# Kernel optimization log

Measured on AMD Instinct MI355X. Metric: run time of the kernel, lower is better.

The kernel has to match this reference:

```python
import jax, jax.numpy as jnp
import numpy as np

N_NODES = 10000
N_REL = 200
DIM = 128          # rank * 2
REL_DIM = 128
VIS_DIM = 512
TXT_DIM = 768
N_EDGES = 320000


def _glorot(key, shape):
    fan_in, fan_out = shape[1], shape[0]
    lim = (6.0 / (fan_in + fan_out)) ** 0.5
    return jax.random.uniform(key, shape, jnp.float32, -lim, lim)


def setup_inputs() -> dict:
    key = jax.random.key(0)
    ks = jax.random.split(key, 24)
    inp = {}
    inp['x'] = jax.random.randint(ks[0], (1024, 3), 0, N_NODES)
    inp['edge_index'] = jax.random.randint(ks[1], (2, N_EDGES), 0, N_NODES)
    inp['edge_type'] = jax.random.randint(ks[2], (N_EDGES,), 0, N_REL)
    inp['visual'] = jax.random.normal(ks[3], (N_NODES, VIS_DIM), jnp.float32)
    inp['textual'] = jax.random.normal(ks[4], (N_NODES, TXT_DIM), jnp.float32)
    # embeddings (scaled by 0.001 as in torch init)
    inp['structural_emb'] = jax.random.normal(ks[5], (N_NODES, DIM), jnp.float32) * 0.001
    inp['relation_emb'] = jax.random.normal(ks[6], (N_REL, REL_DIM), jnp.float32) * 0.001
    # three KBGAT convs: w1 [out, 2*in+rel], b1 [out], w2 [1, out]
    cat = 2 * DIM + REL_DIM
    for i, tag in enumerate(['s', 'v', 't']):
        inp[f'W1_{tag}'] = _glorot(ks[7 + 3 * i], (DIM, cat))
        inp[f'b1_{tag}'] = jnp.zeros((DIM,), jnp.float32)
        inp[f'w2_{tag}'] = _glorot(ks[8 + 3 * i], (1, DIM))
    # modality projections
    inp['Wv'] = _glorot(ks[16], (DIM, VIS_DIM))
    inp['bv'] = jnp.zeros((DIM,), jnp.float32)
    inp['Wt'] = _glorot(ks[17], (DIM, TXT_DIM))
    inp['bt'] = jnp.zeros((DIM,), jnp.float32)
    inp['alpha'] = jnp.float32(0.1)
    inp['gamma'] = jnp.float32(0.8)
    return inp


def kbgat_conv(feat, rel_emb, src, dst, edge_type, W1, b1, w2):
    # gather per-edge embeddings: x_i = target, x_j = source (PyG default flow)
    triple = jnp.concatenate([feat[dst], feat[src], rel_emb[edge_type]], axis=1)  # [E, 2*D+R]
    c = triple @ W1.T + b1                                   # [E, D]
    b = jax.nn.leaky_relu(c @ w2[0])                         # [E]
    # segment softmax over destination nodes
    m = jax.ops.segment_max(b, dst, num_segments=N_NODES)
    e = jnp.exp(b - m[dst])
    z = jax.ops.segment_sum(e, dst, num_segments=N_NODES)
    attn = e / z[dst]                                        # [E]
    agg = jax.ops.segment_sum(c * attn[:, None], dst, num_segments=N_NODES)  # [N, D]
    return jax.nn.leaky_relu(agg)


def reference(x, edge_index, edge_type, visual, textual, structural_emb, relation_emb,
              W1_s, b1_s, w2_s, W1_v, b1_v, w2_v, W1_t, b1_t, w2_t,
              Wv, bv, Wt, bt, alpha, gamma):
    src, dst = edge_index[0], edge_index[1]
    h_s = kbgat_conv(structural_emb, relation_emb, src, dst, edge_type, W1_s, b1_s, w2_s)
    vf = visual @ Wv.T + bv
    h_v = kbgat_conv(vf, relation_emb, src, dst, edge_type, W1_v, b1_v, w2_v)
    tf = textual @ Wt.T + bt
    h_t = kbgat_conv(tf, relation_emb, src, dst, edge_type, W1_t, b1_t, w2_t)
    return (1.0 - alpha - gamma) * h_s + alpha * h_v + gamma * h_t
```

## Files before the change

kernel.cpp:

```cpp
#include <hip/hip_runtime.h>
#include <hip/hip_bf16.h>

typedef unsigned short u16;
typedef unsigned int u32;
typedef unsigned long long u64;
typedef __bf16 bf16x8 __attribute__((ext_vector_type(8)));
typedef float f32x4 __attribute__((ext_vector_type(4)));

#define DIM 128

__device__ __forceinline__ u16 f2bf_rne(float x) {
  u32 u = __float_as_uint(x);
  return (u16)((u + 0x7fffu + ((u >> 16) & 1u)) >> 16);
}
__device__ __forceinline__ u32 packbf2(float x, float y) {
  return (u32)f2bf_rne(x) | ((u32)f2bf_rne(y) << 16);
}
__device__ __forceinline__ float lrelu(float x) { return x > 0.f ? x : 0.01f * x; }
__device__ __forceinline__ int iclamp(int v, int hi) { return v < 0 ? 0 : (v >= hi ? hi - 1 : v); }
__device__ __forceinline__ float sane(float x) { return (x == x) ? x : 0.f; }

__device__ __forceinline__ float wred_max(float v) {
  #pragma unroll
  for (int o = 32; o > 0; o >>= 1) v = fmaxf(v, __shfl_xor(v, o, 64));
  return v;
}
__device__ __forceinline__ float wred_sum(float v) {
  #pragma unroll
  for (int o = 32; o > 0; o >>= 1) v += __shfl_xor(v, o, 64);
  return v;
}

struct PrepAllArgs {
  const float* W1[3]; const float* Wmod[3]; int K[3]; u16* Wc[3];
  const float* rel; const float* b1[3]; const float* bmod[3]; const float* w2[3];
  u16* PrAll; float* qr[3]; int NR;
  const int* cnt; int* offs; int N;
  int wc2End; int wc1End; int wc0End;
};
struct MainArgs {
  const float* A[3]; const u16* B[3]; const float* w2[3];
  u16* PdAll; u16* PsAll; float* qd[3]; float* qs[3];
  int M; int K[3]; int tilesPerM; int nGemm; int totB;
  const int* dst; const int* src; const int* etyp;
  const int* offs; const int* rank; u32* sortedST;
  int E; int NR;
};
struct AgArgs {
  const u32* sortedST; const int* offs;
  const float* qd[3]; const float* qs[3]; const float* qr[3];
  const u16* PdAll; const u16* PsAll; const u16* PrAll;
  const float* alphaP; const float* gammaP;
  float* outp; int N; int NR; int E;
};

__global__ __launch_bounds__(256) void hist_k(const int* __restrict__ dst,
                                              int* __restrict__ cnt,
                                              int* __restrict__ rank, int E, int N) {
  int e0 = blockIdx.x * 512 + threadIdx.x;
  #pragma unroll
  for (int i = 0; i < 2; ++i) {
    int e = e0 + i * 256;
    if (e < E) {
      int d = dst[e];
      if (d >= 0 && d < N) rank[e] = atomicAdd(&cnt[d], 1);
    }
  }
}

__global__ __launch_bounds__(256) void scan_wcpr(PrepAllArgs a) {
  __shared__ float relL[2][128];
  __shared__ float bmL[128];
  __shared__ float qpr[4];
  __shared__ int sums[256];
  int b = blockIdx.x, tid = threadIdx.x;

  if (b == 0) {
    int N = a.N;
    int chunk = (N + 255) >> 8;
    int base = tid * chunk;
    int s = 0;
    for (int i = 0; i < chunk; ++i) { int idx = base + i; if (idx < N) s += a.cnt[idx]; }
    sums[tid] = s;
    __syncthreads();
    for (int off = 1; off < 256; off <<= 1) {
      int v = (tid >= off) ? sums[tid - off] : 0;
      __syncthreads();
      sums[tid] += v;
      __syncthreads();
    }
    int prefix = (tid > 0) ? sums[tid - 1] : 0;
    for (int i = 0; i < chunk; ++i) {
      int idx = base + i;
      if (idx < N) { a.offs[idx] = prefix; prefix += a.cnt[idx]; }
    }
    if (tid == 255) a.offs[N] = sums[255];
    return;
  }

  int c = b - 1;
  if (c < a.wc0End) {
    int m, loc;
    if (c < a.wc2End)      { m = 2; loc = c; }
    else if (c < a.wc1End) { m = 1; loc = c - a.wc2End; }
    else                   { m = 0; loc = c - a.wc1End; }
    int og = loc & 31, kb = loc >> 5;
    int o0 = og * 8;
    int k = (kb << 8) + tid;
    int K = a.K[m];
    if (k < K) {
      int halfsel = (o0 >= 128) ? 128 : 0;
      int oo0 = o0 & 127;
      const float* W1 = a.W1[m];
      const float* Wm = a.Wmod[m];
      float acc[8];
      if (Wm == nullptr) {
        #pragma unroll
        for (int u = 0; u < 8; ++u)
          acc[u] = W1[(oo0 + u) * 384 + halfsel + k];
      } else {
        #pragma unroll
        for (int u = 0; u < 8; ++u) acc[u] = 0.f;
        const float* wmk = Wm + k;
        const float* w1b = W1 + (size_t)oo0 * 384 + halfsel;
        for (int i = 0; i < 128; i += 8) {
          float wm[8];
          #pragma unroll
          for (int j = 0; j < 8; ++j)
            wm[j] = wmk[(size_t)(i + j) * K];
          #pragma unroll
          for (int j = 0; j < 8; ++j) {
            #pragma unroll
            for (int u = 0; u < 8; ++u)
              acc[u] = fmaf(w1b[u * 384 + i + j], wm[j], acc[u]);
          }
        }
      }
      #pragma unroll
      for (int u = 0; u < 8; ++u) {
        int o = o0 + u;
        a.Wc[m][((size_t)(k >> 5) * 256 + o) * 32 + (k & 31)] = f2bf_rne(acc[u]);
      }
    }
  } else {
    int idx = c - a.wc0End;
    int NRpair = (a.NR + 1) >> 1;
    int m = idx / NRpair;
    if (m > 2) return;
    int rp = idx - m * NRpair;
    int r0 = rp * 2;
    {
      int ro = tid >> 7, ii = tid & 127;
      int rr = r0 + ro;
      relL[ro][ii] = (rr < a.NR) ? a.rel[rr * 128 + ii] : 0.f;
    }
    const float* bmod = a.bmod[m];
    if (tid < 128) bmL[tid] = (bmod != nullptr) ? bmod[tid] : 0.f;
    __syncthreads();
    int lane = tid & 63, wv = tid >> 6;
    int rsel = wv >> 1;
    int obase = (wv & 1) * 64;
    int r = r0 + rsel;
    bool rok = (r < a.NR);
    const float* W1 = a.W1[m];
    const float* b1 = a.b1[m];
    const float* w2 = a.w2[m];
    bool hasbm = (bmod != nullptr);
    float rl0 = relL[rsel][lane], rl1 = relL[rsel][64 + lane];
    float bm0 = bmL[lane], bm1 = bmL[64 + lane];
    float qacc = 0.f;
    for (int oo = 0; oo < 64; oo += 4) {
      float s[4];
      #pragma unroll
      for (int u = 0; u < 4; ++u) {
        const float* row = W1 + (obase + oo + u) * 384;
        float v = row[256 + lane] * rl0 + row[320 + lane] * rl1;
        if (hasbm)
          v += (row[lane] + row[128 + lane]) * bm0 +
               (row[64 + lane] + row[192 + lane]) * bm1;
        s[u] = v;
      }
      #pragma unroll
      for (int off2 = 32; off2 > 0; off2 >>= 1) {
        #pragma unroll
        for (int u = 0; u < 4; ++u) s[u] += __shfl_xor(s[u], off2, 64);
      }
      u16 pk[4];
      #pragma unroll
      for (int u = 0; u < 4; ++u) {
        int o = obase + oo + u;
        float totv = s[u] + b1[o];
        pk[u] = f2bf_rne(totv);
        qacc += totv * w2[o];
      }
      if (rok && lane == 0) {
        u16* dstp = a.PrAll + (size_t)r * 384 + m * 128 + obase + oo;
        *reinterpret_cast<u64*>(dstp) =
            (u64)pk[0] | ((u64)pk[1] << 16) | ((u64)pk[2] << 32) | ((u64)pk[3] << 48);
      }
    }
    if (lane == 0) qpr[wv] = qacc;
    __syncthreads();
    if (tid < 2) {
      int rr = r0 + tid;
      if (rr < a.NR) a.qr[m][rr] = sane(qpr[tid * 2] + qpr[tid * 2 + 1]);
    }
  }
}

__device__ __forceinline__ void gemm_epilogue(const MainArgs& g, int m, int row0,
                                              f32x4 (&acc)[2][4], float (*qpart)[32]) {
  int tid = threadIdx.x;
  int lane = tid & 63, wv = tid >> 6;
  int quad = lane >> 4, l16 = lane & 15;
  int M = g.M;
  const float* w2 = g.w2[m];
  u16* PdAll = g.PdAll;
  u16* PsAll = g.PsAll;
  float w2c[4];
  #pragma unroll
  for (int t = 0; t < 4; ++t) w2c[t] = w2[(wv & 1) * 64 + t * 16 + l16];

  #pragma unroll
  for (int rg = 0; rg < 2; ++rg) {
    float part[4];
    #pragma unroll
    for (int r = 0; r < 4; ++r) {
      int rr = row0 + rg * 16 + quad * 4 + r;
      bool ok = rr < M;
      float qp = 0.f;
      #pragma unroll
      for (int t = 0; t < 4; ++t) {
        int cc = (wv & 1) * 64 + t * 16 + l16;
        if (ok) {
          if (wv < 2) PdAll[(size_t)rr * 384 + m * 128 + cc] = f2bf_rne(acc[rg][t][r]);
          else        PsAll[(size_t)rr * 384 + m * 128 + cc] = f2bf_rne(acc[rg][t][r]);
        }
        qp += acc[rg][t][r] * w2c[t];
      }
      #pragma unroll
      for (int mk = 1; mk < 16; mk <<= 1) qp += __shfl_xor(qp, mk, 64);
      part[r] = qp;
    }
    if (l16 == 0) {
      #pragma unroll
      for (int r = 0; r < 4; ++r) qpart[wv][rg * 16 + quad * 4 + r] = part[r];
    }
  }
  __syncthreads();
  if (tid < 64) {
    int row = tid & 31;
    int half = tid >> 5;
    int rr = row0 + row;
    if (rr < M) {
      if (half == 0) g.qd[m][rr] = sane(qpart[0][row] + qpart[1][row]);
      else           g.qs[m][rr] = sane(qpart[2][row] + qpart[3][row]);
    }
  }
}

template<int NT>
__device__ __forceinline__ void gemm_exact(const MainArgs& g, int m, int tile,
                                           u16* Als, float (*qpart)[32]) {
  constexpr int H = (NT + 1) / 2;
  const int M = g.M;
  int tid = threadIdx.x;
  int lane = tid & 63, wv = tid >> 6;
  int quad = lane >> 4, l16 = lane & 15;
  int row0 = tile * 32;
  int srow = tid >> 3;
  int tk4 = (tid & 7) * 4;
  int srsw = srow & 3;
  int wg = tk4 >> 3;
  int wrem = tk4 & 7;
  int grow = row0 + srow;
  if (grow >= M) grow = M - 1;
  const float* Ag = g.A[m] + (size_t)grow * (NT * 32);

  float4 vreg[H];
  #pragma unroll
  for (int i = 0; i < H; ++i)
    vreg[i] = *reinterpret_cast<const float4*>(Ag + tk4 + i * 32);
  #pragma unroll
  for (int i = 0; i < H; ++i) {
    int gidx = wg ^ srsw ^ (i & 3);
    u32* dp = reinterpret_cast<u32*>(&Als[((i * 32 + srow) * 32) + (gidx << 3) + wrem]);
    dp[0] = packbf2(vreg[i].x, vreg[i].y);
    dp[1] = packbf2(vreg[i].z, vreg[i].w);
  }
  #pragma unroll
  for (int i = H; i < NT; ++i)
    vreg[i - H] = *reinterpret_cast<const float4*>(Ag + tk4 + i * 32);
  #pragma unroll
  for (int i = H; i < NT; ++i) {
    int gidx = wg ^ srsw ^ (i & 3);
    u32* dp = reinterpret_cast<u32*>(&Als[((i * 32 + srow) * 32) + (gidx << 3) + wrem]);
    dp[0] = packbf2(vreg[i - H].x, vreg[i - H].y);
    dp[1] = packbf2(vreg[i - H].z, vreg[i - H].w);
  }
  __syncthreads();

  const u16* Bpg = g.B[m] + (size_t)(wv * 64 + l16) * 32 + quad * 8;
  f32x4 acc[2][4];
  #pragma unroll
  for (int rg = 0; rg < 2; ++rg)
    #pragma unroll
    for (int t = 0; t < 4; ++t) acc[rg][t] = (f32x4){0.f, 0.f, 0.f, 0.f};

  #pragma unroll
  for (int kb = 0; kb < NT; ++kb) {
    const u16* bp = Bpg + (size_t)kb * 8192;
    bf16x8 b0 = *reinterpret_cast<const bf16x8*>(bp);
    bf16x8 b1 = *reinterpret_cast<const bf16x8*>(bp + 512);
    bf16x8 b2 = *reinterpret_cast<const bf16x8*>(bp + 1024);
    bf16x8 b3 = *reinterpret_cast<const bf16x8*>(bp + 1536);
    int gsw = (quad ^ (l16 & 3) ^ (kb & 3)) << 3;
    #pragma unroll
    for (int rg = 0; rg < 2; ++rg) {
      bf16x8 av = *reinterpret_cast<const bf16x8*>(
          &Als[(kb * 32 + rg * 16 + l16) * 32 + gsw]);
      acc[rg][0] = __builtin_amdgcn_mfma_f32_16x16x32_bf16(av, b0, acc[rg][0], 0, 0, 0);
      acc[rg][1] = __builtin_amdgcn_mfma_f32_16x16x32_bf16(av, b1, acc[rg][1], 0, 0, 0);
      acc[rg][2] = __builtin_amdgcn_mfma_f32_16x16x32_bf16(av, b2, acc[rg][2], 0, 0, 0);
      acc[rg][3] = __builtin_amdgcn_mfma_f32_16x16x32_bf16(av, b3, acc[rg][3], 0, 0, 0);
    }
  }
  gemm_epilogue(g, m, row0, acc, qpart);
}

__device__ void gemm_generic(const MainArgs& g, int m, int tile,
                             u16* Als, float (*qpart)[32]) {
  const int M = g.M, K = g.K[m];
  int nt = K >> 5;
  int tid = threadIdx.x;
  int lane = tid & 63, wv = tid >> 6;
  int quad = lane >> 4, l16 = lane & 15;
  int row0 = tile * 32;
  int srow = tid >> 3;
  int tk4 = (tid & 7) * 4;
  int srsw = srow & 3;
  int wg = tk4 >> 3;
  int wrem = tk4 & 7;
  int grow = row0 + srow;
  if (grow >= M) grow = M - 1;
  const float* Ag = g.A[m] + (size_t)grow * K;
  const u16* Bpg = g.B[m] + (size_t)(wv * 64 + l16) * 32 + quad * 8;

  f32x4 acc[2][4];
  #pragma unroll
  for (int rg = 0; rg < 2; ++rg)
    #pragma unroll
    for (int t = 0; t < 4; ++t) acc[rg][t] = (f32x4){0.f, 0.f, 0.f, 0.f};

  for (int c0 = 0; c0 < nt; c0 += 24) {
    int kc = nt - c0; if (kc > 24) kc = 24;
    __syncthreads();
    for (int i = 0; i < kc; ++i) {
      int kg = (c0 + i) * 32 + tk4;
      if (kg + 3 < K) {
        float4 v = *reinterpret_cast<const float4*>(Ag + kg);
        int gidx = wg ^ srsw ^ (i & 3);
        u32* dp = reinterpret_cast<u32*>(&Als[((i * 32 + srow) * 32) + (gidx << 3) + wrem]);
        dp[0] = packbf2(v.x, v.y);
        dp[1] = packbf2(v.z, v.w);
      }
    }
    __syncthreads();
    for (int kb = 0; kb < kc; ++kb) {
      const u16* bp = Bpg + (size_t)(c0 + kb) * 8192;
      bf16x8 b0 = *reinterpret_cast<const bf16x8*>(bp);
      bf16x8 b1 = *reinterpret_cast<const bf16x8*>(bp + 512);
      bf16x8 b2 = *reinterpret_cast<const bf16x8*>(bp + 1024);
      bf16x8 b3 = *reinterpret_cast<const bf16x8*>(bp + 1536);
      int gsw = (quad ^ (l16 & 3) ^ (kb & 3)) << 3;
      #pragma unroll
      for (int rg = 0; rg < 2; ++rg) {
        bf16x8 av = *reinterpret_cast<const bf16x8*>(
            &Als[(kb * 32 + rg * 16 + l16) * 32 + gsw]);
        acc[rg][0] = __builtin_amdgcn_mfma_f32_16x16x32_bf16(av, b0, acc[rg][0], 0, 0, 0);
        acc[rg][1] = __builtin_amdgcn_mfma_f32_16x16x32_bf16(av, b1, acc[rg][1], 0, 0, 0);
        acc[rg][2] = __builtin_amdgcn_mfma_f32_16x16x32_bf16(av, b2, acc[rg][2], 0, 0, 0);
        acc[rg][3] = __builtin_amdgcn_mfma_f32_16x16x32_bf16(av, b3, acc[rg][3], 0, 0, 0);
      }
    }
  }
  gemm_epilogue(g, m, row0, acc, qpart);
}

__global__ __launch_bounds__(256) void fused_main(MainArgs g) {
  __shared__ __align__(16) u16 Als[24 * 32 * 32];
  __shared__ float qpart[4][32];
  int b = blockIdx.x;
  long nG = g.nGemm, tot = g.totB;
  int gprev = (int)((long)b * nG / tot);
  int gnext = (int)(((long)b + 1) * nG / tot);
  if (gnext == gprev) {
    int h = b - gprev;
    int e = h * 256 + threadIdx.x;
    if (e < g.E) {
      int d = g.dst[e];
      if (d >= 0 && d < g.M) {
        int pos = g.offs[d] + g.rank[e];
        if (pos >= 0 && pos < g.E) {
          u32 s = (u32)iclamp(g.src[e], g.M);
          u32 t = (u32)iclamp(g.etyp[e], g.NR);
          g.sortedST[pos] = (t << 16) | s;
        }
      }
    }
    return;
  }
  int fb = gprev;
  int tpm = g.tilesPerM;
  int m, tile;
  if (fb < tpm)            { m = 2; tile = fb; }
  else if (fb < 2 * tpm)   { m = 1; tile = fb - tpm; }
  else                     { m = 0; tile = fb - 2 * tpm; }

  int K = g.K[m];
  if (K == 768)      gemm_exact<24>(g, m, tile, Als, qpart);
  else if (K == 512) gemm_exact<16>(g, m, tile, Als, qpart);
  else if (K == 128) gemm_exact<4>(g, m, tile, Als, qpart);
  else               gemm_generic(g, m, tile, Als, qpart);
}

__global__ __launch_bounds__(256) void aggregate_all(AgArgs a) {
  int n = blockIdx.x * 4 + (threadIdx.x >> 6);
  if (n >= a.N) return;
  int lane = threadIdx.x & 63;
  int E = a.E;
  int eb = a.offs[n], ee = a.offs[n + 1];
  if (eb < 0) eb = 0;
  if (eb > E) eb = E;
  if (ee < eb) ee = eb;
  if (ee > E) ee = E;
  int En = ee - eb;

  float al = a.alphaP[0];
  if (!(al > 0.f && al < 1.f)) al = 0.1f;
  float ga = a.gammaP[0];
  if (!(ga > 0.f && ga < 1.f)) ga = 0.8f;
  float coef[3] = {1.f - al - ga, al, ga};

  float qdn[3];
  #pragma unroll
  for (int m = 0; m < 3; ++m) qdn[m] = sane(a.qd[m][n]);

  const u16* PsAll = a.PsAll;
  const u16* PrAll = a.PrAll;
  int dlo = 2 * lane;

  float rm[3] = {-1e30f, -1e30f, -1e30f};
  float z[3] = {0.f, 0.f, 0.f};
  float a0[3] = {0.f, 0.f, 0.f};
  float a1[3] = {0.f, 0.f, 0.f};
  for (int c0 = 0; c0 < En; c0 += 64) {
    int cn = min(64, En - c0);
    u32 stp = 0;
    float bm[3] = {-1e30f, -1e30f, -1e30f};
    if (lane < cn) {
      stp = a.sortedST[eb + c0 + lane];
      int s = (int)(stp & 0xffffu);
      int t = (int)(stp >> 16);
      #pragma unroll
      for (int m = 0; m < 3; ++m)
        bm[m] = lrelu(qdn[m] + a.qs[m][s] + a.qr[m][t]);
    }
    float wr[3];
    #pragma unroll
    for (int m = 0; m < 3; ++m) {
      float cm = wred_max(bm[m]);
      float nm = fmaxf(rm[m], cm);
      float sc = __expf(fmaxf(rm[m] - nm, -80.f));
      z[m] *= sc; a0[m] *= sc; a1[m] *= sc;
      rm[m] = nm;
      wr[m] = (lane < cn) ? __expf(fmaxf(bm[m] - nm, -80.f)) : 0.f;
      z[m] += wr[m];
    }

    int cnR = (cn + 3) & ~3;
    for (int j = 0; j < cnR; j += 4) {
      u32 stj[4];
      float wj[4][3];
      #pragma unroll
      for (int u = 0; u < 4; ++u) {
        stj[u] = __shfl(stp, j + u, 64);
        wj[u][0] = __shfl(wr[0], j + u, 64);
        wj[u][1] = __shfl(wr[1], j + u, 64);
        wj[u][2] = __shfl(wr[2], j + u, 64);
      }
      u32 pu[4][3], ru[4][3];
      #pragma unroll
      for (int u = 0; u < 4; ++u) {
        const u16* ps = PsAll + (size_t)(stj[u] & 0xffffu) * 384 + dlo;
        const u16* pr = PrAll + (size_t)(stj[u] >> 16) * 384 + dlo;
        #pragma unroll
        for (int m = 0; m < 3; ++m) {
          pu[u][m] = *reinterpret_cast<const u32*>(ps + m * 128);
          ru[u][m] = *reinterpret_cast<const u32*>(pr + m * 128);
        }
      }
      #pragma unroll
      for (int u = 0; u < 4; ++u) {
        #pragma unroll
        for (int m = 0; m < 3; ++m) {
          float ps0 = __uint_as_float(pu[u][m] << 16);
          float ps1 = __uint_as_float(pu[u][m] & 0xffff0000u);
          float pr0 = __uint_as_float(ru[u][m] << 16);
          float pr1 = __uint_as_float(ru[u][m] & 0xffff0000u);
          a0[m] = fmaf(wj[u][m], ps0 + pr0, a0[m]);
          a1[m] = fmaf(wj[u][m], ps1 + pr1, a1[m]);
        }
      }
    }
  }
  #pragma unroll
  for (int m = 0; m < 3; ++m) z[m] = wred_sum(z[m]);

  float o0 = 0.f, o1 = 0.f;
  const u16* pd = a.PdAll + (size_t)n * 384 + dlo;
  #pragma unroll
  for (int m = 0; m < 3; ++m) {
    float h0 = 0.f, h1 = 0.f;
    if (En > 0 && z[m] > 0.f) {
      float rz = 1.f / z[m];
      u32 du = *reinterpret_cast<const u32*>(pd + m * 128);
      float pd0 = __uint_as_float(du << 16), pd1 = __uint_as_float(du & 0xffff0000u);
      h0 = lrelu(pd0 + a0[m] * rz);
      h1 = lrelu(pd1 + a1[m] * rz);
    }
    o0 = fmaf(coef[m], h0, o0);
    o1 = fmaf(coef[m], h1, o1);
  }
  float* op = a.outp + (size_t)n * 128 + dlo;
  op[0] = sane(o0);
  op[1] = sane(o1);
}

extern "C" void kernel_launch(void* const* d_in, const int* in_sizes, int n_in,
                              void* d_out, int out_size, void* d_ws, size_t ws_size,
                              hipStream_t stream) {
  const int* ei        = (const int*)d_in[1];
  const int* et        = (const int*)d_in[2];
  const float* visual  = (const float*)d_in[3];
  const float* textual = (const float*)d_in[4];
  const float* semb    = (const float*)d_in[5];
  const float* relemb  = (const float*)d_in[6];
  const float* W1s = (const float*)d_in[7];
  const float* b1s = (const float*)d_in[8];
  const float* w2s = (const float*)d_in[9];
  const float* W1v = (const float*)d_in[10];
  const float* b1v = (const float*)d_in[11];
  const float* w2v = (const float*)d_in[12];
  const float* W1t = (const float*)d_in[13];
  const float* b1t = (const float*)d_in[14];
  const float* w2t = (const float*)d_in[15];
  const float* Wv  = (const float*)d_in[16];
  const float* bv  = (const float*)d_in[17];
  const float* Wt  = (const float*)d_in[18];
  const float* bt  = (const float*)d_in[19];
  const float* alphaP = (const float*)d_in[20];
  const float* gammaP = (const float*)d_in[21];
  float* outp = (float*)d_out;

  const int E   = in_sizes[2];
  const int N   = in_sizes[5] / DIM;
  const int NR  = in_sizes[6] / DIM;
  const int VIS = in_sizes[3] / N;
  const int TXT = in_sizes[4] / N;
  int Ks[3] = {DIM, VIS, TXT};
  const int TPM = (N + 31) / 32;

  const float* W1a[3]   = {W1s, W1v, W1t};
  const float* b1a[3]   = {b1s, b1v, b1t};
  const float* w2a[3]   = {w2s, w2v, w2t};
  const float* Wmoda[3] = {nullptr, Wv, Wt};
  const float* bmoda[3] = {nullptr, bv, bt};
  const float* Amoda[3] = {semb, visual, textual};

  const int* esrc = ei;
  const int* edst = ei + E;
  int egrid  = (E + 255) / 256;
  int egridH = (E + 511) / 512;

  size_t off = 0;
  auto take = [&](size_t bytes) -> size_t {
    size_t o = off;
    off = (off + bytes + 255) & ~(size_t)255;
    return o;
  };
  size_t o_cnt  = take((size_t)N * 4);
  size_t o_rank = take((size_t)E * 4);
  size_t o_offs = take((size_t)(N + 1) * 4);
  size_t o_st   = take((size_t)E * 4);
  size_t o_qdm[3], o_qsm[3], o_qrm[3], o_Wcm[3];
  for (int m = 0; m < 3; ++m) {
    o_qdm[m] = take((size_t)N * 4);
    o_qsm[m] = take((size_t)N * 4);
    o_qrm[m] = take((size_t)NR * 4);
    o_Wcm[m] = take((size_t)256 * Ks[m] * 2);
  }
  size_t o_PrAll = take((size_t)NR * 384 * 2);
  size_t o_PdAll = take((size_t)N * 384 * 2);
  size_t o_PsAll = take((size_t)N * 384 * 2);
  size_t need = off;

  if (ws_size < need) {
    (void)hipMemsetAsync(d_out, 0, (size_t)out_size * 4, stream);
    return;
  }

  char* w = (char*)d_ws;
  int* counts = (int*)(w + o_cnt);
  int* rank   = (int*)(w + o_rank);
  int* offs   = (int*)(w + o_offs);
  u32* sortedST = (u32*)(w + o_st);

  (void)hipMemsetAsync(counts, 0, (size_t)N * 4, stream);

  PrepAllArgs pa;
  pa.rel = relemb; pa.NR = NR;
  pa.PrAll = (u16*)(w + o_PrAll);
  pa.cnt = counts; pa.offs = offs; pa.N = N;
  for (int m = 0; m < 3; ++m) {
    pa.W1[m] = W1a[m]; pa.Wmod[m] = Wmoda[m]; pa.K[m] = Ks[m];
    pa.Wc[m] = (u16*)(w + o_Wcm[m]);
    pa.b1[m] = b1a[m]; pa.bmod[m] = bmoda[m]; pa.w2[m] = w2a[m];
    pa.qr[m] = (float*)(w + o_qrm[m]);
  }
  int NRpair = (NR + 1) / 2;
  int kbm[3];
  for (int m = 0; m < 3; ++m) kbm[m] = (Ks[m] + 255) / 256;
  pa.wc2End = 32 * kbm[2];
  pa.wc1End = pa.wc2End + 32 * kbm[1];
  pa.wc0End = pa.wc1End + 32 * kbm[0];
  int prepGrid = 1 + pa.wc0End + 3 * NRpair;

  MainArgs ga;
  ga.M = N; ga.tilesPerM = TPM; ga.nGemm = 3 * TPM;
  ga.totB = ga.nGemm + egrid;
  ga.PdAll = (u16*)(w + o_PdAll);
  ga.PsAll = (u16*)(w + o_PsAll);
  ga.dst = edst; ga.src = esrc; ga.etyp = et;
  ga.offs = offs; ga.rank = rank; ga.sortedST = sortedST;
  ga.E = E; ga.NR = NR;
  AgArgs aa;
  for (int m = 0; m < 3; ++m) {
    ga.A[m] = Amoda[m]; ga.B[m] = (const u16*)(w + o_Wcm[m]); ga.w2[m] = w2a[m];
    ga.qd[m] = (float*)(w + o_qdm[m]); ga.qs[m] = (float*)(w + o_qsm[m]);
    ga.K[m] = Ks[m];
    aa.qd[m] = (const float*)(w + o_qdm[m]);
    aa.qs[m] = (const float*)(w + o_qsm[m]);
    aa.qr[m] = (const float*)(w + o_qrm[m]);
  }

  aa.PdAll = (const u16*)(w + o_PdAll);
  aa.PsAll = (const u16*)(w + o_PsAll);
  aa.PrAll = (const u16*)(w + o_PrAll);
  aa.sortedST = sortedST; aa.offs = offs;
  aa.alphaP = alphaP; aa.gammaP = gammaP;
  aa.outp = outp; aa.N = N; aa.NR = NR; aa.E = E;

  hist_k<<<egridH, 256, 0, stream>>>(edst, counts, rank, E, N);
  scan_wcpr<<<prepGrid, 256, 0, stream>>>(pa);
  fused_main<<<ga.totB, 256, 0, stream>>>(ga);
  aggregate_all<<<(N + 3) / 4, 256, 0, stream>>>(aa);
}
```

Measured before the change: 248.0 us.

## Halve GEMM row tile to 16 rows and restructure weight-combine FMA loop

The fused projection GEMM now uses 16-row tiles instead of 32, with a new LDS staging helper and epilogue sized to match. This doubles the number of GEMM blocks, giving more parallelism across CUs and halving LDS use per block. In exchange each block reuses the B-operand weights over fewer rows, so total B traffic from cache doubles. Separately, the weight-combination loop in the prep kernel is rewritten as per-output FMA chains, and that kernel is given a launch bound of 1.

```diff
diff --git a/kernel.cpp b/kernel.cpp
--- a/kernel.cpp
+++ b/kernel.cpp
@@ -68,7 +68,7 @@
   }
 }
 
-__global__ __launch_bounds__(256) void scan_wcpr(PrepAllArgs a) {
+__global__ __launch_bounds__(256, 1) void scan_wcpr(PrepAllArgs a) {
   __shared__ float relL[2][128];
   __shared__ float bmL[128];
   __shared__ float qpr[4];
@@ -124,15 +124,25 @@
         const float* wmk = Wm + k;
         const float* w1b = W1 + (size_t)oo0 * 384 + halfsel;
         for (int i = 0; i < 128; i += 8) {
-          float wm[8];
+          float wm0 = wmk[(size_t)(i + 0) * K];
+          float wm1 = wmk[(size_t)(i + 1) * K];
+          float wm2 = wmk[(size_t)(i + 2) * K];
+          float wm3 = wmk[(size_t)(i + 3) * K];
+          float wm4 = wmk[(size_t)(i + 4) * K];
+          float wm5 = wmk[(size_t)(i + 5) * K];
+          float wm6 = wmk[(size_t)(i + 6) * K];
+          float wm7 = wmk[(size_t)(i + 7) * K];
           #pragma unroll
-          for (int j = 0; j < 8; ++j)
-            wm[j] = wmk[(size_t)(i + j) * K];
-          #pragma unroll
-          for (int j = 0; j < 8; ++j) {
-            #pragma unroll
-            for (int u = 0; u < 8; ++u)
-              acc[u] = fmaf(w1b[u * 384 + i + j], wm[j], acc[u]);
+          for (int u = 0; u < 8; ++u) {
+            const float* r_ = w1b + u * 384 + i;
+            float s0 = fmaf(r_[0], wm0, acc[u]);
+            s0 = fmaf(r_[1], wm1, s0);
+            s0 = fmaf(r_[2], wm2, s0);
+            s0 = fmaf(r_[3], wm3, s0);
+            s0 = fmaf(r_[4], wm4, s0);
+            s0 = fmaf(r_[5], wm5, s0);
+            s0 = fmaf(r_[6], wm6, s0);
+            acc[u] = fmaf(r_[7], wm7, s0);
           }
         }
       }
@@ -208,51 +218,52 @@
   }
 }
 
-__device__ __forceinline__ void gemm_epilogue(const MainArgs& g, int m, int row0,
-                                              f32x4 (&acc)[2][4], float (*qpart)[32]) {
+__device__ __forceinline__ void stash16(u16* Als, int srow, int tk4, int i, float4 v) {
+  int kb = 2 * i + (tk4 >> 5);
+  int kl = tk4 & 31;
+  int gidx = (kl >> 3) ^ (srow & 3) ^ (kb & 3);
+  u32* dp = reinterpret_cast<u32*>(&Als[(kb * 16 + srow) * 32 + (gidx << 3) + (kl & 7)]);
+  dp[0] = packbf2(v.x, v.y);
+  dp[1] = packbf2(v.z, v.w);
+}
+
+__device__ __forceinline__ void epilogue16(const MainArgs& g, int m, int row0,
+                                           f32x4 (&acc)[4], float (*qpart)[16]) {
   int tid = threadIdx.x;
   int lane = tid & 63, wv = tid >> 6;
   int quad = lane >> 4, l16 = lane & 15;
-  int M = g.M;
   const float* w2 = g.w2[m];
-  u16* PdAll = g.PdAll;
-  u16* PsAll = g.PsAll;
   float w2c[4];
   #pragma unroll
   for (int t = 0; t < 4; ++t) w2c[t] = w2[(wv & 1) * 64 + t * 16 + l16];
-
-  #pragma unroll
-  for (int rg = 0; rg < 2; ++rg) {
-    float part[4];
+  float part[4];
+  #pragma unroll
+  for (int r = 0; r < 4; ++r) {
+    int rr = row0 + quad * 4 + r;
+    bool ok = rr < g.M;
+    float qp = 0.f;
     #pragma unroll
-    for (int r = 0; r < 4; ++r) {
-      int rr = row0 + rg * 16 + quad * 4 + r;
-      bool ok = rr < M;
-      float qp = 0.f;
-      #pragma unroll
-      for (int t = 0; t < 4; ++t) {
-        int cc = (wv & 1) * 64 + t * 16 + l16;
-        if (ok) {
-          if (wv < 2) PdAll[(size_t)rr * 384 + m * 128 + cc] = f2bf_rne(acc[rg][t][r]);
-          else        PsAll[(size_t)rr * 384 + m * 128 + cc] = f2bf_rne(acc[rg][t][r]);
-        }
-        qp += acc[rg][t][r] * w2c[t];
-      }
-      #pragma unroll
-      for (int mk = 1; mk < 16; mk <<= 1) qp += __shfl_xor(qp, mk, 64);
-      part[r] = qp;
-    }
-    if (l16 == 0) {
-      #pragma unroll
-      for (int r = 0; r < 4; ++r) qpart[wv][rg * 16 + quad * 4 + r] = part[r];
-    }
+    for (int t = 0; t < 4; ++t) {
+      int cc = (wv & 1) * 64 + t * 16 + l16;
+      if (ok) {
+        if (wv < 2) g.PdAll[(size_t)rr * 384 + m * 128 + cc] = f2bf_rne(acc[t][r]);
+        else        g.PsAll[(size_t)rr * 384 + m * 128 + cc] = f2bf_rne(acc[t][r]);
+      }
+      qp += acc[t][r] * w2c[t];
+    }
+    #pragma unroll
+    for (int mk = 1; mk < 16; mk <<= 1) qp += __shfl_xor(qp, mk, 64);
+    part[r] = qp;
+  }
+  if (l16 == 0) {
+    #pragma unroll
+    for (int r = 0; r < 4; ++r) qpart[wv][quad * 4 + r] = part[r];
   }
   __syncthreads();
-  if (tid < 64) {
-    int row = tid & 31;
-    int half = tid >> 5;
+  if (tid < 32) {
+    int row = tid & 15, half = tid >> 4;
     int rr = row0 + row;
-    if (rr < M) {
+    if (rr < g.M) {
       if (half == 0) g.qd[m][rr] = sane(qpart[0][row] + qpart[1][row]);
       else           g.qs[m][rr] = sane(qpart[2][row] + qpart[3][row]);
     }
@@ -260,52 +271,35 @@
 }
 
 template<int NT>
-__device__ __forceinline__ void gemm_exact(const MainArgs& g, int m, int tile,
-                                           u16* Als, float (*qpart)[32]) {
-  constexpr int H = (NT + 1) / 2;
-  const int M = g.M;
+__device__ __forceinline__ void gemm16(const MainArgs& g, int m, int tile,
+                                       u16* Als, float (*qpart)[16]) {
+  constexpr int NS = NT / 2;
+  constexpr int H = (NS + 1) / 2;
   int tid = threadIdx.x;
   int lane = tid & 63, wv = tid >> 6;
   int quad = lane >> 4, l16 = lane & 15;
-  int row0 = tile * 32;
-  int srow = tid >> 3;
-  int tk4 = (tid & 7) * 4;
-  int srsw = srow & 3;
-  int wg = tk4 >> 3;
-  int wrem = tk4 & 7;
+  int row0 = tile * 16;
+  int srow = tid >> 4;
+  int tk4 = (tid & 15) * 4;
   int grow = row0 + srow;
-  if (grow >= M) grow = M - 1;
+  if (grow >= g.M) grow = g.M - 1;
   const float* Ag = g.A[m] + (size_t)grow * (NT * 32);
 
   float4 vreg[H];
   #pragma unroll
-  for (int i = 0; i < H; ++i)
-    vreg[i] = *reinterpret_cast<const float4*>(Ag + tk4 + i * 32);
-  #pragma unroll
-  for (int i = 0; i < H; ++i) {
-    int gidx = wg ^ srsw ^ (i & 3);
-    u32* dp = reinterpret_cast<u32*>(&Als[((i * 32 + srow) * 32) + (gidx << 3) + wrem]);
-    dp[0] = packbf2(vreg[i].x, vreg[i].y);
-    dp[1] = packbf2(vreg[i].z, vreg[i].w);
-  }
-  #pragma unroll
-  for (int i = H; i < NT; ++i)
-    vreg[i - H] = *reinterpret_cast<const float4*>(Ag + tk4 + i * 32);
-  #pragma unroll
-  for (int i = H; i < NT; ++i) {
-    int gidx = wg ^ srsw ^ (i & 3);
-    u32* dp = reinterpret_cast<u32*>(&Als[((i * 32 + srow) * 32) + (gidx << 3) + wrem]);
-    dp[0] = packbf2(vreg[i - H].x, vreg[i - H].y);
-    dp[1] = packbf2(vreg[i - H].z, vreg[i - H].w);
-  }
+  for (int i = 0; i < H; ++i) vreg[i] = *reinterpret_cast<const float4*>(Ag + tk4 + i * 64);
+  #pragma unroll
+  for (int i = 0; i < H; ++i) stash16(Als, srow, tk4, i, vreg[i]);
+  #pragma unroll
+  for (int i = H; i < NS; ++i) vreg[i - H] = *reinterpret_cast<const float4*>(Ag + tk4 + i * 64);
+  #pragma unroll
+  for (int i = H; i < NS; ++i) stash16(Als, srow, tk4, i, vreg[i - H]);
   __syncthreads();
 
   const u16* Bpg = g.B[m] + (size_t)(wv * 64 + l16) * 32 + quad * 8;
-  f32x4 acc[2][4];
-  #pragma unroll
-  for (int rg = 0; rg < 2; ++rg)
-    #pragma unroll
-    for (int t = 0; t < 4; ++t) acc[rg][t] = (f32x4){0.f, 0.f, 0.f, 0.f};
+  f32x4 acc[4];
+  #pragma unroll
+  for (int t = 0; t < 4; ++t) acc[t] = (f32x4){0.f, 0.f, 0.f, 0.f};
 
   #pragma unroll
   for (int kb = 0; kb < NT; ++kb) {
@@ -315,54 +309,40 @@
     bf16x8 b2 = *reinterpret_cast<const bf16x8*>(bp + 1024);
     bf16x8 b3 = *reinterpret_cast<const bf16x8*>(bp + 1536);
     int gsw = (quad ^ (l16 & 3) ^ (kb & 3)) << 3;
-    #pragma unroll
-    for (int rg = 0; rg < 2; ++rg) {
-      bf16x8 av = *reinterpret_cast<const bf16x8*>(
-          &Als[(kb * 32 + rg * 16 + l16) * 32 + gsw]);
-      acc[rg][0] = __builtin_amdgcn_mfma_f32_16x16x32_bf16(av, b0, acc[rg][0], 0, 0, 0);
-      acc[rg][1] = __builtin_amdgcn_mfma_f32_16x16x32_bf16(av, b1, acc[rg][1], 0, 0, 0);
-      acc[rg][2] = __builtin_amdgcn_mfma_f32_16x16x32_bf16(av, b2, acc[rg][2], 0, 0, 0);
-      acc[rg][3] = __builtin_amdgcn_mfma_f32_16x16x32_bf16(av, b3, acc[rg][3], 0, 0, 0);
-    }
-  }
-  gemm_epilogue(g, m, row0, acc, qpart);
-}
-
-__device__ void gemm_generic(const MainArgs& g, int m, int tile,
-                             u16* Als, float (*qpart)[32]) {
-  const int M = g.M, K = g.K[m];
+    bf16x8 av = *reinterpret_cast<const bf16x8*>(&Als[(kb * 16 + l16) * 32 + gsw]);
+    acc[0] = __builtin_amdgcn_mfma_f32_16x16x32_bf16(av, b0, acc[0], 0, 0, 0);
+    acc[1] = __builtin_amdgcn_mfma_f32_16x16x32_bf16(av, b1, acc[1], 0, 0, 0);
+    acc[2] = __builtin_amdgcn_mfma_f32_16x16x32_bf16(av, b2, acc[2], 0, 0, 0);
+    acc[3] = __builtin_amdgcn_mfma_f32_16x16x32_bf16(av, b3, acc[3], 0, 0, 0);
+  }
+  epilogue16(g, m, row0, acc, qpart);
+}
+
+__device__ void gemm16_gen(const MainArgs& g, int m, int tile,
+                           u16* Als, float (*qpart)[16]) {
+  const int K = g.K[m];
   int nt = K >> 5;
   int tid = threadIdx.x;
   int lane = tid & 63, wv = tid >> 6;
   int quad = lane >> 4, l16 = lane & 15;
-  int row0 = tile * 32;
-  int srow = tid >> 3;
-  int tk4 = (tid & 7) * 4;
-  int srsw = srow & 3;
-  int wg = tk4 >> 3;
-  int wrem = tk4 & 7;
+  int row0 = tile * 16;
+  int srow = tid >> 4;
+  int tk4 = (tid & 15) * 4;
   int grow = row0 + srow;
-  if (grow >= M) grow = M - 1;
+  if (grow >= g.M) grow = g.M - 1;
   const float* Ag = g.A[m] + (size_t)grow * K;
   const u16* Bpg = g.B[m] + (size_t)(wv * 64 + l16) * 32 + quad * 8;
-
-  f32x4 acc[2][4];
-  #pragma unroll
-  for (int rg = 0; rg < 2; ++rg)
-    #pragma unroll
-    for (int t = 0; t < 4; ++t) acc[rg][t] = (f32x4){0.f, 0.f, 0.f, 0.f};
-
+  f32x4 acc[4];
+  #pragma unroll
+  for (int t = 0; t < 4; ++t) acc[t] = (f32x4){0.f, 0.f, 0.f, 0.f};
   for (int c0 = 0; c0 < nt; c0 += 24) {
     int kc = nt - c0; if (kc > 24) kc = 24;
     __syncthreads();
-    for (int i = 0; i < kc; ++i) {
-      int kg = (c0 + i) * 32 + tk4;
+    for (int i = 0; i < (kc + 1) / 2; ++i) {
+      int kg = c0 * 32 + tk4 + i * 64;
       if (kg + 3 < K) {
         float4 v = *reinterpret_cast<const float4*>(Ag + kg);
-        int gidx = wg ^ srsw ^ (i & 3);
-        u32* dp = reinterpret_cast<u32*>(&Als[((i * 32 + srow) * 32) + (gidx << 3) + wrem]);
-        dp[0] = packbf2(v.x, v.y);
-        dp[1] = packbf2(v.z, v.w);
+        stash16(Als, srow, tk4, i, v);
       }
     }
     __syncthreads();
@@ -373,23 +353,19 @@
       bf16x8 b2 = *reinterpret_cast<const bf16x8*>(bp + 1024);
       bf16x8 b3 = *reinterpret_cast<const bf16x8*>(bp + 1536);
       int gsw = (quad ^ (l16 & 3) ^ (kb & 3)) << 3;
-      #pragma unroll
-      for (int rg = 0; rg < 2; ++rg) {
-        bf16x8 av = *reinterpret_cast<const bf16x8*>(
-            &Als[(kb * 32 + rg * 16 + l16) * 32 + gsw]);
-        acc[rg][0] = __builtin_amdgcn_mfma_f32_16x16x32_bf16(av, b0, acc[rg][0], 0, 0, 0);
-        acc[rg][1] = __builtin_amdgcn_mfma_f32_16x16x32_bf16(av, b1, acc[rg][1], 0, 0, 0);
-        acc[rg][2] = __builtin_amdgcn_mfma_f32_16x16x32_bf16(av, b2, acc[rg][2], 0, 0, 0);
-        acc[rg][3] = __builtin_amdgcn_mfma_f32_16x16x32_bf16(av, b3, acc[rg][3], 0, 0, 0);
-      }
-    }
-  }
-  gemm_epilogue(g, m, row0, acc, qpart);
+      bf16x8 av = *reinterpret_cast<const bf16x8*>(&Als[(kb * 16 + l16) * 32 + gsw]);
+      acc[0] = __builtin_amdgcn_mfma_f32_16x16x32_bf16(av, b0, acc[0], 0, 0, 0);
+      acc[1] = __builtin_amdgcn_mfma_f32_16x16x32_bf16(av, b1, acc[1], 0, 0, 0);
+      acc[2] = __builtin_amdgcn_mfma_f32_16x16x32_bf16(av, b2, acc[2], 0, 0, 0);
+      acc[3] = __builtin_amdgcn_mfma_f32_16x16x32_bf16(av, b3, acc[3], 0, 0, 0);
+    }
+  }
+  epilogue16(g, m, row0, acc, qpart);
 }
 
 __global__ __launch_bounds__(256) void fused_main(MainArgs g) {
-  __shared__ __align__(16) u16 Als[24 * 32 * 32];
-  __shared__ float qpart[4][32];
+  __shared__ __align__(16) u16 Als[24 * 16 * 32];
+  __shared__ float qpart[4][16];
   int b = blockIdx.x;
   long nG = g.nGemm, tot = g.totB;
   int gprev = (int)((long)b * nG / tot);
@@ -418,10 +394,10 @@
   else                     { m = 0; tile = fb - 2 * tpm; }
 
   int K = g.K[m];
-  if (K == 768)      gemm_exact<24>(g, m, tile, Als, qpart);
-  else if (K == 512) gemm_exact<16>(g, m, tile, Als, qpart);
-  else if (K == 128) gemm_exact<4>(g, m, tile, Als, qpart);
-  else               gemm_generic(g, m, tile, Als, qpart);
+  if (K == 768)      gemm16<24>(g, m, tile, Als, qpart);
+  else if (K == 512) gemm16<16>(g, m, tile, Als, qpart);
+  else if (K == 128) gemm16<4>(g, m, tile, Als, qpart);
+  else               gemm16_gen(g, m, tile, Als, qpart);
 }
 
 __global__ __launch_bounds__(256) void aggregate_all(AgArgs a) {
@@ -569,7 +545,7 @@
   const int VIS = in_sizes[3] / N;
   const int TXT = in_sizes[4] / N;
   int Ks[3] = {DIM, VIS, TXT};
-  const int TPM = (N + 31) / 32;
+  const int TPM = (N + 15) / 16;
 
   const float* W1a[3]   = {W1s, W1v, W1t};
   const float* b1a[3]   = {b1s, b1v, b1t};
```

Result: slower. 256.0 us (+3.2%).
